# Kernel tuning notes

Measured on AMD Instinct MI355X. Metric: run time of the kernel, lower is better.

## Reference

```python
import jax, jax.numpy as jnp
import numpy as np
import math

EPS = 1e-6


def setup_inputs() -> dict:
    key = jax.random.key(0)
    k1, k2 = jax.random.split(key)
    B, S, D, F = 4, 4096, 2048, 2048
    x = jax.random.normal(k1, (B, S, D), dtype=jnp.float32)
    weight = jax.random.normal(k2, (F, D), dtype=jnp.float32) / np.sqrt(D)
    alpha = jnp.ones((1,), dtype=jnp.float32)
    bias = jnp.zeros((F,), dtype=jnp.float32)
    return {"x": x, "weight": weight, "alpha": alpha, "bias": bias}


def reference(x, weight, alpha, bias):
    F = weight.shape[0]
    # y: [B, S, F]
    y = jnp.einsum("bsd,fd->bsf", x, weight)
    x_sq = jnp.sum(x * x, axis=-1, keepdims=True)        # [B, S, 1]
    w_sq = jnp.sum(weight * weight, axis=-1)              # [F]
    distances = x_sq + w_sq - 2.0 * y                     # squared Euclidean dist
    out = (y * y) / (distances + EPS)
    scale = (math.sqrt(F) / math.log(1.0 + F)) ** alpha   # alpha shape (1,) broadcasts
    out = out * scale + bias
    return out
```

## Files before the change

kernel.cpp:

```cpp
#include <hip/hip_runtime.h>
#include <hip/hip_bf16.h>
#include <cstdint>
#include <cstddef>


typedef __bf16 bf16_t;
typedef __bf16 bf16x8 __attribute__((ext_vector_type(8)));
typedef __bf16 bf16x4 __attribute__((ext_vector_type(4)));
typedef float f32x4 __attribute__((ext_vector_type(4)));

constexpr int M_DIM = 16384;
constexpr int N_DIM = 2048;
constexpr int K_DIM = 2048;
constexpr int BM = 256, BN = 128, BK = 32;
constexpr int KITERS = K_DIM / BK;

__device__ __forceinline__ void async16(const bf16_t* g, bf16_t* l) {
    __builtin_amdgcn_global_load_lds(
        (const __attribute__((address_space(1))) void*)g,
        (__attribute__((address_space(3))) void*)l,
        16, 0, 0);
}

__global__ __launch_bounds__(256) void prep_convert(const float* __restrict__ x,
                                                    const float* __restrict__ w,
                                                    bf16_t* __restrict__ xb,
                                                    bf16_t* __restrict__ wb,
                                                    float* __restrict__ xsq,
                                                    float* __restrict__ wsq) {
    const int row = blockIdx.x;
    const float* src;
    bf16_t* dstb;
    float* dsts;
    if (row < M_DIM) {
        src = x + (size_t)row * K_DIM;
        dstb = xb + (size_t)row * K_DIM;
        dsts = xsq + row;
    } else {
        const int r = row - M_DIM;
        src = w + (size_t)r * K_DIM;
        dstb = wb + (size_t)r * K_DIM;
        dsts = wsq + r;
    }
    const float4* s4 = (const float4*)src;
    const float4 a = s4[threadIdx.x];
    const float4 b = s4[threadIdx.x + 256];
    float s = a.x * a.x + a.y * a.y + a.z * a.z + a.w * a.w
            + b.x * b.x + b.y * b.y + b.z * b.z + b.w * b.w;
    bf16x4 av = { (bf16_t)a.x, (bf16_t)a.y, (bf16_t)a.z, (bf16_t)a.w };
    bf16x4 bv = { (bf16_t)b.x, (bf16_t)b.y, (bf16_t)b.z, (bf16_t)b.w };
    ((bf16x4*)dstb)[threadIdx.x] = av;
    ((bf16x4*)dstb)[threadIdx.x + 256] = bv;
#pragma unroll
    for (int off = 32; off > 0; off >>= 1) s += __shfl_down(s, off, 64);
    __shared__ float red[4];
    const int lane = threadIdx.x & 63;
    const int wv = threadIdx.x >> 6;
    if (lane == 0) red[wv] = s;
    __syncthreads();
    if (threadIdx.x == 0) *dsts = red[0] + red[1] + red[2] + red[3];
}

__global__ __launch_bounds__(512, 4) void yat_gemm(const bf16_t* __restrict__ A,
                                                   const bf16_t* __restrict__ Bw,
                                                   const float* __restrict__ xsq,
                                                   const float* __restrict__ wsq,
                                                   const float* __restrict__ bias,
                                                   const float* __restrict__ alpha,
                                                   float* __restrict__ out) {
    __shared__ bf16_t As[BM * BK];
    __shared__ bf16_t Bs[BN * BK];

    const int tid = threadIdx.x;
    const int lane = tid & 63;
    const int wv = tid >> 6;
    const int wm = wv >> 1;
    const int wn = wv & 1;

    const int bm = (int)blockIdx.x >> 4;
    const int bn = (int)blockIdx.x & 15;

    const int srow = wv * 16 + (lane >> 2);
    const int gch = (lane & 3) ^ ((lane >> 3) & 3);
    const bf16_t* Ag = A + ((size_t)(bm * BM + srow)) * K_DIM + gch * 8;
    const bf16_t* Bg = Bw + ((size_t)(bn * BN + srow)) * K_DIM + gch * 8;
    bf16_t* ldsA = As + srow * BK + (lane & 3) * 8;
    bf16_t* ldsB = Bs + srow * BK + (lane & 3) * 8;

    const int frm = lane & 15;
    const int jch = lane >> 4;
    const int sw = (lane >> 1) & 3;
    const int choff = ((jch ^ sw) * 8);

    f32x4 acc[4][4] = {};

    for (int kt = 0; kt < KITERS; ++kt) {
        const int k0 = kt * BK;
        async16(Ag + k0, ldsA);
        async16(Ag + k0 + (size_t)128 * K_DIM, ldsA + 128 * BK);
        async16(Bg + k0, ldsB);
        __syncthreads();

        bf16x8 af[4], bv[4];
#pragma unroll
        for (int i = 0; i < 4; ++i)
            af[i] = *(const bf16x8*)&As[(wm * 64 + i * 16 + frm) * BK + choff];
#pragma unroll
        for (int j = 0; j < 4; ++j)
            bv[j] = *(const bf16x8*)&Bs[(wn * 64 + j * 16 + frm) * BK + choff];
#pragma unroll
        for (int i = 0; i < 4; ++i)
#pragma unroll
            for (int j = 0; j < 4; ++j)
                acc[i][j] = __builtin_amdgcn_mfma_f32_16x16x32_bf16(af[i], bv[j], acc[i][j], 0, 0, 0);
        __syncthreads();
    }

    const float sc = powf(sqrtf((float)N_DIM) / logf(1.0f + (float)N_DIM), alpha[0]);
    float wsq_c[4], bias_c[4];
#pragma unroll
    for (int j = 0; j < 4; ++j) {
        const int col = bn * BN + wn * 64 + j * 16 + frm;
        wsq_c[j] = wsq[col];
        bias_c[j] = bias[col];
    }
#pragma unroll
    for (int i = 0; i < 4; ++i) {
#pragma unroll
        for (int r = 0; r < 4; ++r) {
            const int row = bm * BM + wm * 64 + i * 16 + (lane >> 4) * 4 + r;
            const float xs = xsq[row];
            float* orow = out + (size_t)row * N_DIM + bn * BN + wn * 64 + frm;
#pragma unroll
            for (int j = 0; j < 4; ++j) {
                const float y = acc[i][j][r];
                const float d = xs + wsq_c[j] - 2.0f * y + 1e-6f;
                orow[j * 16] = (y * y) / d * sc + bias_c[j];
            }
        }
    }
}

extern "C" void kernel_launch(void* const* d_in, const int* in_sizes, int n_in,
                              void* d_out, int out_size, void* d_ws, size_t ws_size,
                              hipStream_t stream) {
    (void)in_sizes; (void)n_in; (void)out_size; (void)ws_size;
    const float* x = (const float*)d_in[0];
    const float* w = (const float*)d_in[1];
    const float* alpha = (const float*)d_in[2];
    const float* bias = (const float*)d_in[3];
    float* out = (float*)d_out;

    bf16_t* xb = (bf16_t*)d_ws;
    bf16_t* wb = xb + (size_t)M_DIM * K_DIM;
    float* xsq = (float*)(wb + (size_t)N_DIM * K_DIM);
    float* wsq = xsq + M_DIM;

    prep_convert<<<M_DIM + N_DIM, 256, 0, stream>>>(x, w, xb, wb, xsq, wsq);
    yat_gemm<<<(M_DIM / BM) * (N_DIM / BN), 512, 0, stream>>>(xb, wb, xsq, wsq, bias, alpha, out);
}
```

Measured before the change: 386.6 us.

## Enlarge GEMM tile to 256x256x64 with 8-wave ping-pong LDS pipeline

```diff
diff --git a/kernel.cpp b/kernel.cpp
--- a/kernel.cpp
+++ b/kernel.cpp
@@ -12,8 +12,9 @@
 constexpr int M_DIM = 16384;
 constexpr int N_DIM = 2048;
 constexpr int K_DIM = 2048;
-constexpr int BM = 256, BN = 128, BK = 32;
-constexpr int KITERS = K_DIM / BK;
+constexpr int BM = 256, BN = 256, BK = 64;
+constexpr int KT = K_DIM / BK;
+constexpr int SEG = 128 * 64;
 
 __device__ __forceinline__ void async16(const bf16_t* g, bf16_t* l) {
     __builtin_amdgcn_global_load_lds(
@@ -61,60 +62,108 @@
     if (threadIdx.x == 0) *dsts = red[0] + red[1] + red[2] + red[3];
 }
 
-__global__ __launch_bounds__(512, 4) void yat_gemm(const bf16_t* __restrict__ A,
+__global__ __launch_bounds__(512, 2) void yat_gemm(const bf16_t* __restrict__ A,
                                                    const bf16_t* __restrict__ Bw,
                                                    const float* __restrict__ xsq,
                                                    const float* __restrict__ wsq,
                                                    const float* __restrict__ bias,
                                                    const float* __restrict__ alpha,
                                                    float* __restrict__ out) {
-    __shared__ bf16_t As[BM * BK];
-    __shared__ bf16_t Bs[BN * BK];
-
-    const int tid = threadIdx.x;
+    __shared__ bf16_t sA[4 * SEG];
+    __shared__ bf16_t sB[4 * SEG];
+
+    const int tid = (int)threadIdx.x;
     const int lane = tid & 63;
     const int wv = tid >> 6;
-    const int wm = wv >> 1;
-    const int wn = wv & 1;
-
-    const int bm = (int)blockIdx.x >> 4;
-    const int bn = (int)blockIdx.x & 15;
-
-    const int srow = wv * 16 + (lane >> 2);
-    const int gch = (lane & 3) ^ ((lane >> 3) & 3);
-    const bf16_t* Ag = A + ((size_t)(bm * BM + srow)) * K_DIM + gch * 8;
-    const bf16_t* Bg = Bw + ((size_t)(bn * BN + srow)) * K_DIM + gch * 8;
-    bf16_t* ldsA = As + srow * BK + (lane & 3) * 8;
-    bf16_t* ldsB = Bs + srow * BK + (lane & 3) * 8;
+    const int wm = wv >> 2;
+    const int wn = wv & 3;
+
+    const int bm = (int)blockIdx.x >> 3;
+    const int bn = (int)blockIdx.x & 7;
 
     const int frm = lane & 15;
     const int jch = lane >> 4;
-    const int sw = (lane >> 1) & 3;
-    const int choff = ((jch ^ sw) * 8);
-
-    f32x4 acc[4][4] = {};
-
-    for (int kt = 0; kt < KITERS; ++kt) {
-        const int k0 = kt * BK;
-        async16(Ag + k0, ldsA);
-        async16(Ag + k0 + (size_t)128 * K_DIM, ldsA + 128 * BK);
-        async16(Bg + k0, ldsB);
-        __syncthreads();
-
-        bf16x8 af[4], bv[4];
-#pragma unroll
-        for (int i = 0; i < 4; ++i)
-            af[i] = *(const bf16x8*)&As[(wm * 64 + i * 16 + frm) * BK + choff];
-#pragma unroll
-        for (int j = 0; j < 4; ++j)
-            bv[j] = *(const bf16x8*)&Bs[(wn * 64 + j * 16 + frm) * BK + choff];
-#pragma unroll
-        for (int i = 0; i < 4; ++i)
-#pragma unroll
-            for (int j = 0; j < 4; ++j)
-                acc[i][j] = __builtin_amdgcn_mfma_f32_16x16x32_bf16(af[i], bv[j], acc[i][j], 0, 0, 0);
-        __syncthreads();
-    }
+    const int sx = frm & 7;
+
+    const int st_r = tid >> 3;
+    const int st_g = (tid & 7) ^ (st_r & 7);
+    const bf16_t* Ast = A + (size_t)(bm * BM + st_r) * K_DIM + st_g * 8;
+    const bf16_t* Bst = Bw + (size_t)(bn * BN + st_r) * K_DIM + st_g * 8;
+
+    auto stageA = [&](int kt, int h) {
+        if (kt >= KT) return;
+        bf16_t* d = sA + ((kt * 2 + h) & 3) * SEG + tid * 8;
+        const bf16_t* s = Ast + (size_t)(h * 128) * K_DIM + kt * 64;
+        async16(s, d);
+        async16(s + (size_t)64 * K_DIM, d + 4096);
+    };
+    auto stageB = [&](int kt, int h) {
+        if (kt >= KT) return;
+        bf16_t* d = sB + ((kt * 2 + h) & 3) * SEG + tid * 8;
+        const bf16_t* s = Bst + (size_t)(h * 128) * K_DIM + kt * 64;
+        async16(s, d);
+        async16(s + (size_t)64 * K_DIM, d + 4096);
+    };
+
+    f32x4 acc[8][4] = {};
+    bf16x8 bfr[4][2];
+
+    stageB(0, 0); stageB(0, 1);
+    stageA(0, 0); stageA(0, 1);
+    stageB(1, 0); stageB(1, 1);
+    asm volatile("s_waitcnt vmcnt(4)" ::: "memory");
+    asm volatile("s_barrier" ::: "memory");
+
+#define PHASE(Q, KTT, SMAT, SKT, SH, VMEND)                                     \
+    {                                                                           \
+        if ((Q) == 0) {                                                         \
+            const int bslot = (((KTT) * 2 + (wn >> 1)) & 3) * SEG;              \
+            _Pragma("unroll") for (int j = 0; j < 4; ++j) {                     \
+                const int brow = (wn & 1) * 64 + j * 16 + frm;                  \
+                _Pragma("unroll") for (int kk = 0; kk < 2; ++kk)                \
+                    bfr[j][kk] = *(const bf16x8*)&sB[bslot + brow * 64 +        \
+                                                    (((kk * 4 + jch) ^ sx) * 8)]; \
+            }                                                                   \
+        }                                                                       \
+        bf16x8 af[2][2];                                                        \
+        {                                                                       \
+            const int aslot = (((KTT) * 2 + wm) & 3) * SEG;                     \
+            _Pragma("unroll") for (int i2 = 0; i2 < 2; ++i2) {                  \
+                const int arow = ((Q) * 2 + i2) * 16 + frm;                     \
+                _Pragma("unroll") for (int kk = 0; kk < 2; ++kk)                \
+                    af[i2][kk] = *(const bf16x8*)&sA[aslot + arow * 64 +        \
+                                                    (((kk * 4 + jch) ^ sx) * 8)]; \
+            }                                                                   \
+        }                                                                       \
+        if ((SMAT) == 0) stageA((SKT), (SH)); else stageB((SKT), (SH));         \
+        asm volatile("s_barrier" ::: "memory");                                 \
+        __builtin_amdgcn_s_setprio(1);                                          \
+        _Pragma("unroll") for (int kk = 0; kk < 2; ++kk)                        \
+            _Pragma("unroll") for (int i2 = 0; i2 < 2; ++i2)                    \
+                _Pragma("unroll") for (int j = 0; j < 4; ++j)                   \
+                    acc[(Q) * 2 + i2][j] = __builtin_amdgcn_mfma_f32_16x16x32_bf16( \
+                        af[i2][kk], bfr[j][kk], acc[(Q) * 2 + i2][j], 0, 0, 0); \
+        __builtin_amdgcn_s_setprio(0);                                          \
+        if (VMEND) {                                                            \
+            if ((SKT) >= KT) { asm volatile("s_waitcnt vmcnt(0)" ::: "memory"); } \
+            else             { asm volatile("s_waitcnt vmcnt(4)" ::: "memory"); } \
+        }                                                                       \
+        asm volatile("s_barrier" ::: "memory");                                 \
+    }
+
+#pragma unroll 1
+    for (int u = 0; u < KT / 2; ++u) {
+        const int a = 2 * u, b = 2 * u + 1;
+        PHASE(0, a, 0, b,     0, 0)
+        PHASE(1, a, 0, b,     1, 0)
+        PHASE(2, a, 1, a + 2, 0, 0)
+        PHASE(3, a, 1, a + 2, 1, 1)
+        PHASE(0, b, 0, a + 2, 0, 0)
+        PHASE(1, b, 0, a + 2, 1, 0)
+        PHASE(2, b, 1, b + 2, 0, 0)
+        PHASE(3, b, 1, b + 2, 1, 1)
+    }
+#undef PHASE
 
     const float sc = powf(sqrtf((float)N_DIM) / logf(1.0f + (float)N_DIM), alpha[0]);
     float wsq_c[4], bias_c[4];
@@ -125,10 +174,10 @@
         bias_c[j] = bias[col];
     }
 #pragma unroll
-    for (int i = 0; i < 4; ++i) {
+    for (int i = 0; i < 8; ++i) {
 #pragma unroll
         for (int r = 0; r < 4; ++r) {
-            const int row = bm * BM + wm * 64 + i * 16 + (lane >> 4) * 4 + r;
+            const int row = bm * BM + wm * 128 + i * 16 + jch * 4 + r;
             const float xs = xsq[row];
             float* orow = out + (size_t)row * N_DIM + bn * BN + wn * 64 + frm;
 #pragma unroll
```

Result: faster. 359.5 us (-7.0%).

## Use 256x256 tiles with triple-buffered async LDS pipeline and wave-per-row prep

Applied to the files above, without the earlier changes.

```diff
diff --git a/kernel.cpp b/kernel.cpp
--- a/kernel.cpp
+++ b/kernel.cpp
@@ -12,8 +12,9 @@
 constexpr int M_DIM = 16384;
 constexpr int N_DIM = 2048;
 constexpr int K_DIM = 2048;
-constexpr int BM = 256, BN = 128, BK = 32;
-constexpr int KITERS = K_DIM / BK;
+constexpr int BM = 256, BN = 256, BK = 32;
+constexpr int KT = K_DIM / BK;
+constexpr int SEG = 128 * 32;
 
 __device__ __forceinline__ void async16(const bf16_t* g, bf16_t* l) {
     __builtin_amdgcn_global_load_lds(
@@ -28,93 +29,152 @@
                                                     bf16_t* __restrict__ wb,
                                                     float* __restrict__ xsq,
                                                     float* __restrict__ wsq) {
-    const int row = blockIdx.x;
-    const float* src;
-    bf16_t* dstb;
-    float* dsts;
-    if (row < M_DIM) {
-        src = x + (size_t)row * K_DIM;
-        dstb = xb + (size_t)row * K_DIM;
-        dsts = xsq + row;
-    } else {
-        const int r = row - M_DIM;
-        src = w + (size_t)r * K_DIM;
-        dstb = wb + (size_t)r * K_DIM;
-        dsts = wsq + r;
-    }
-    const float4* s4 = (const float4*)src;
-    const float4 a = s4[threadIdx.x];
-    const float4 b = s4[threadIdx.x + 256];
-    float s = a.x * a.x + a.y * a.y + a.z * a.z + a.w * a.w
-            + b.x * b.x + b.y * b.y + b.z * b.z + b.w * b.w;
-    bf16x4 av = { (bf16_t)a.x, (bf16_t)a.y, (bf16_t)a.z, (bf16_t)a.w };
-    bf16x4 bv = { (bf16_t)b.x, (bf16_t)b.y, (bf16_t)b.z, (bf16_t)b.w };
-    ((bf16x4*)dstb)[threadIdx.x] = av;
-    ((bf16x4*)dstb)[threadIdx.x + 256] = bv;
-#pragma unroll
-    for (int off = 32; off > 0; off >>= 1) s += __shfl_down(s, off, 64);
-    __shared__ float red[4];
     const int lane = threadIdx.x & 63;
     const int wv = threadIdx.x >> 6;
-    if (lane == 0) red[wv] = s;
-    __syncthreads();
-    if (threadIdx.x == 0) *dsts = red[0] + red[1] + red[2] + red[3];
-}
-
-__global__ __launch_bounds__(512, 4) void yat_gemm(const bf16_t* __restrict__ A,
+    const int base = blockIdx.x * 8 + wv * 2;
+#pragma unroll
+    for (int it = 0; it < 2; ++it) {
+        const int row = base + it;
+        const float* src;
+        bf16_t* dstb;
+        float* dsts;
+        if (row < M_DIM) {
+            src = x + (size_t)row * K_DIM;
+            dstb = xb + (size_t)row * K_DIM;
+            dsts = xsq + row;
+        } else {
+            const int r = row - M_DIM;
+            src = w + (size_t)r * K_DIM;
+            dstb = wb + (size_t)r * K_DIM;
+            dsts = wsq + r;
+        }
+        const float4* s4 = (const float4*)src;
+        bf16x4* d4 = (bf16x4*)dstb;
+        float s = 0.0f;
+#pragma unroll
+        for (int j = 0; j < 8; ++j) {
+            const float4 a = s4[lane + j * 64];
+            s += a.x * a.x + a.y * a.y + a.z * a.z + a.w * a.w;
+            bf16x4 v = { (bf16_t)a.x, (bf16_t)a.y, (bf16_t)a.z, (bf16_t)a.w };
+            d4[lane + j * 64] = v;
+        }
+#pragma unroll
+        for (int off = 32; off > 0; off >>= 1) s += __shfl_down(s, off, 64);
+        if (lane == 0) *dsts = s;
+    }
+}
+
+__global__ __launch_bounds__(512, 2) void yat_gemm(const bf16_t* __restrict__ A,
                                                    const bf16_t* __restrict__ Bw,
                                                    const float* __restrict__ xsq,
                                                    const float* __restrict__ wsq,
                                                    const float* __restrict__ bias,
                                                    const float* __restrict__ alpha,
                                                    float* __restrict__ out) {
-    __shared__ bf16_t As[BM * BK];
-    __shared__ bf16_t Bs[BN * BK];
-
-    const int tid = threadIdx.x;
+    __shared__ bf16_t sA[6 * SEG];
+    __shared__ bf16_t sB[6 * SEG];
+
+    const int tid = (int)threadIdx.x;
     const int lane = tid & 63;
     const int wv = tid >> 6;
-    const int wm = wv >> 1;
-    const int wn = wv & 1;
-
-    const int bm = (int)blockIdx.x >> 4;
-    const int bn = (int)blockIdx.x & 15;
-
-    const int srow = wv * 16 + (lane >> 2);
-    const int gch = (lane & 3) ^ ((lane >> 3) & 3);
-    const bf16_t* Ag = A + ((size_t)(bm * BM + srow)) * K_DIM + gch * 8;
-    const bf16_t* Bg = Bw + ((size_t)(bn * BN + srow)) * K_DIM + gch * 8;
-    bf16_t* ldsA = As + srow * BK + (lane & 3) * 8;
-    bf16_t* ldsB = Bs + srow * BK + (lane & 3) * 8;
+    const int wm = wv >> 2;
+    const int wn = wv & 3;
+    const int bh = wn >> 1;
+
+    const int bm = (int)blockIdx.x >> 3;
+    const int bn = (int)blockIdx.x & 7;
 
     const int frm = lane & 15;
     const int jch = lane >> 4;
-    const int sw = (lane >> 1) & 3;
-    const int choff = ((jch ^ sw) * 8);
-
-    f32x4 acc[4][4] = {};
-
-    for (int kt = 0; kt < KITERS; ++kt) {
-        const int k0 = kt * BK;
-        async16(Ag + k0, ldsA);
-        async16(Ag + k0 + (size_t)128 * K_DIM, ldsA + 128 * BK);
-        async16(Bg + k0, ldsB);
-        __syncthreads();
-
-        bf16x8 af[4], bv[4];
+
+    const int st_r = tid >> 2;
+    const int st_g = (tid & 3) ^ ((tid >> 3) & 3);
+    const bf16_t* Ast = A + (size_t)(bm * BM + st_r) * K_DIM + st_g * 8;
+    const bf16_t* Bst = Bw + (size_t)(bn * BN + st_r) * K_DIM + st_g * 8;
+    const size_t h1off = (size_t)128 * K_DIM;
+
+    f32x4 acc[8][4] = {};
+    bf16x8 af[4], bf[4];
+
+#define AOFF(I) (((I)*16 + frm) * 32 + ((jch ^ ((((I)*16 + frm) >> 1) & 3)) * 8))
+#define BOFF(J) ((bh ? 0 : 0), (((wn & 1) * 64 + (J)*16 + frm) * 32 + \
+                 ((jch ^ ((((wn & 1) * 64 + (J)*16 + frm) >> 1) & 3)) * 8)))
+
+#define SBAR asm volatile("s_barrier" ::: "memory");
+#define LGKM0 asm volatile("s_waitcnt lgkmcnt(0)" ::: "memory");
+#define VM4 asm volatile("s_waitcnt vmcnt(4)" ::: "memory");
+#define VM0 asm volatile("s_waitcnt vmcnt(0)" ::: "memory");
+
+    {
+        async16(Ast, sA + 0 * SEG + tid * 8);
+        async16(Bst, sB + 0 * SEG + tid * 8);
+        async16(Ast + h1off, sA + 1 * SEG + tid * 8);
+        async16(Bst + h1off, sB + 1 * SEG + tid * 8);
+        async16(Ast + 32, sA + 2 * SEG + tid * 8);
+        async16(Bst + 32, sB + 2 * SEG + tid * 8);
+        async16(Ast + h1off + 32, sA + 3 * SEG + tid * 8);
+        async16(Bst + h1off + 32, sB + 3 * SEG + tid * 8);
+    }
+    VM4
+    SBAR
+
+    int su = 0;
+#pragma unroll 1
+    for (int u = 0; u < KT; ++u) {
+        const int sv = (su >= 1) ? (su - 1) : (su + 2);
+        const bool st = (u + 2) < KT;
+        const bf16_t* aB = sA + (su * 2 + wm) * SEG;
+        const bf16_t* bB = sB + (su * 2 + bh) * SEG;
+        const bf16_t* Asrc = Ast + (size_t)(u + 2) * 32;
+        const bf16_t* Bsrc = Bst + (size_t)(u + 2) * 32;
+        bf16_t* aD0 = sA + (sv * 2) * SEG + tid * 8;
+        bf16_t* bD0 = sB + (sv * 2) * SEG + tid * 8;
+
+        af[0] = *(const bf16x8*)(aB + AOFF(0));
+        af[1] = *(const bf16x8*)(aB + AOFF(1));
+        af[2] = *(const bf16x8*)(aB + AOFF(2));
+        af[3] = *(const bf16x8*)(aB + AOFF(3));
+        bf[0] = *(const bf16x8*)(bB + BOFF(0));
+        bf[1] = *(const bf16x8*)(bB + BOFF(1));
+        bf[2] = *(const bf16x8*)(bB + BOFF(2));
+        bf[3] = *(const bf16x8*)(bB + BOFF(3));
+        if (st) { async16(Asrc, aD0); async16(Bsrc, bD0); }
+        SBAR
+        LGKM0
+        __builtin_amdgcn_s_setprio(1);
 #pragma unroll
         for (int i = 0; i < 4; ++i)
-            af[i] = *(const bf16x8*)&As[(wm * 64 + i * 16 + frm) * BK + choff];
-#pragma unroll
-        for (int j = 0; j < 4; ++j)
-            bv[j] = *(const bf16x8*)&Bs[(wn * 64 + j * 16 + frm) * BK + choff];
+#pragma unroll
+            for (int j = 0; j < 4; ++j)
+                acc[i][j] = __builtin_amdgcn_mfma_f32_16x16x32_bf16(af[i], bf[j], acc[i][j], 0, 0, 0);
+        __builtin_amdgcn_s_setprio(0);
+        SBAR
+
+        af[0] = *(const bf16x8*)(aB + AOFF(4));
+        af[1] = *(const bf16x8*)(aB + AOFF(5));
+        af[2] = *(const bf16x8*)(aB + AOFF(6));
+        af[3] = *(const bf16x8*)(aB + AOFF(7));
+        if (st) { async16(Asrc + h1off, aD0 + SEG); async16(Bsrc + h1off, bD0 + SEG); }
+        SBAR
+        LGKM0
+        __builtin_amdgcn_s_setprio(1);
 #pragma unroll
         for (int i = 0; i < 4; ++i)
 #pragma unroll
             for (int j = 0; j < 4; ++j)
-                acc[i][j] = __builtin_amdgcn_mfma_f32_16x16x32_bf16(af[i], bv[j], acc[i][j], 0, 0, 0);
-        __syncthreads();
-    }
+                acc[4 + i][j] = __builtin_amdgcn_mfma_f32_16x16x32_bf16(af[i], bf[j], acc[4 + i][j], 0, 0, 0);
+        __builtin_amdgcn_s_setprio(0);
+        if (u < KT - 2) { VM4 } else { VM0 }
+        SBAR
+
+        su = (su == 2) ? 0 : (su + 1);
+    }
+#undef AOFF
+#undef BOFF
+#undef SBAR
+#undef LGKM0
+#undef VM4
+#undef VM0
 
     const float sc = powf(sqrtf((float)N_DIM) / logf(1.0f + (float)N_DIM), alpha[0]);
     float wsq_c[4], bias_c[4];
@@ -125,10 +185,10 @@
         bias_c[j] = bias[col];
     }
 #pragma unroll
-    for (int i = 0; i < 4; ++i) {
+    for (int i = 0; i < 8; ++i) {
 #pragma unroll
         for (int r = 0; r < 4; ++r) {
-            const int row = bm * BM + wm * 64 + i * 16 + (lane >> 4) * 4 + r;
+            const int row = bm * BM + wm * 128 + i * 16 + jch * 4 + r;
             const float xs = xsq[row];
             float* orow = out + (size_t)row * N_DIM + bn * BN + wn * 64 + frm;
 #pragma unroll
@@ -156,6 +216,6 @@
     float* xsq = (float*)(wb + (size_t)N_DIM * K_DIM);
     float* wsq = xsq + M_DIM;
 
-    prep_convert<<<M_DIM + N_DIM, 256, 0, stream>>>(x, w, xb, wb, xsq, wsq);
+    prep_convert<<<(M_DIM + N_DIM) / 8, 256, 0, stream>>>(x, w, xb, wb, xsq, wsq);
     yat_gemm<<<(M_DIM / BM) * (N_DIM / BN), 512, 0, stream>>>(xb, wb, xsq, wsq, bias, alpha, out);
 }
```

Result: no change. 382.2 us (-1.1%).
